# Kernel optimization log

Hardware: AMD Instinct MI355X
Metric: run time of the kernel (lower is better)

Reference implementation:

```python
import jax, jax.numpy as jnp
import numpy as np

C = 128; L = 2; LMAX = 3; NB = 8
R_MAX = 5.0; P_CUT = 5.0; AVG_NEI = 16.0
DELTA_K = 0.2; K_CUT = 0.6; NKRBF = 128; DP = 8
B_GRAPHS = 8; N_ATOMS = 3200; N_EDGES = 51200; NEL = 10
SKIP = (2.0 + 1.0) ** -0.5  # skip_connection_factor with use_ewald=True
_LOFLM_NP = np.repeat(np.arange(4), [1, 3, 5, 7])  # l index of each of 16 lm slots
LOFLM = jnp.asarray(_LOFLM_NP)
LM1H = jnp.asarray(np.eye(4, dtype=np.float32)[_LOFLM_NP])  # [16,4] one-hot lm->l


def _k_grid_np():
    r = np.arange(-3, 4)
    g = np.stack(np.meshgrid(r, r, r, indexing='ij'), -1).reshape(-1, 3).astype(np.float32) * DELTA_K
    return g[np.linalg.norm(g, axis=1) <= K_CUT + 1e-6]  # [K,3], K=123


def _k_rbf_np(kg):
    d = np.linalg.norm(kg, axis=1)
    c = np.linspace(0.0, K_CUT, NKRBF).astype(np.float32)
    w = c[1] - c[0]
    return np.exp(-0.5 * ((d[:, None] - c[None, :]) / w) ** 2).astype(np.float32)


def _sph_harm(u):
    # real spherical harmonics, e3nn 'component' normalization, l=0..3 -> 16 comps
    x, y, z = u[:, 0], u[:, 1], u[:, 2]
    s3, s5, s15 = 3.0 ** 0.5, 5.0 ** 0.5, 15.0 ** 0.5
    c70, c105, c42, c7 = 70.0 ** 0.5 / 4.0, 105.0 ** 0.5, 42.0 ** 0.5 / 4.0, 7.0 ** 0.5 / 2.0
    comps = [jnp.ones_like(x),
             s3 * x, s3 * y, s3 * z,
             s15 * x * y, s15 * y * z, 0.5 * s5 * (3 * z * z - 1.0), s15 * x * z, 0.5 * s15 * (x * x - y * y),
             c70 * y * (3 * x * x - y * y), c105 * x * y * z, c42 * y * (5 * z * z - 1.0),
             c7 * z * (5 * z * z - 3.0), c42 * x * (5 * z * z - 1.0), 0.5 * c105 * z * (x * x - y * y),
             c70 * x * (x * x - 3 * y * y)]
    return jnp.stack(comps, axis=-1)


def _radial(r):
    # Bessel basis * polynomial cutoff envelope (p=5)
    n = jnp.arange(1, NB + 1, dtype=r.dtype)
    rb = jnp.sqrt(2.0 / R_MAX) * jnp.sin(n * jnp.pi * r[:, None] / R_MAX) / jnp.maximum(r, 1e-9)[:, None]
    uu = jnp.clip(r / R_MAX, 0.0, 1.0)
    p = P_CUT
    env = 1.0 - (p + 1.0) * (p + 2.0) / 2.0 * uu ** 5 + p * (p + 2.0) * uu ** 6 - p * (p + 1.0) / 2.0 * uu ** 7
    env = env * (r < R_MAX)
    return rb * env[:, None]


def _forward(positions, node_attrs, shifts, edge_index, batch, kgrid, krbf, W_embed, atomic_E, rW1, rb1, rW2, rb2, rW3, rb3, rW4, Wup, w2, w3, Wmix, Wr0, Wr1a, Wr1b, Wdown, WupE, Wpre1, bpre1, Wpre2, bpre2, Wm1, bm1, Wm2, bm2):
    silu = jax.nn.silu
    src, dst = edge_index[0], edge_index[1]
    vec = positions[dst] - positions[src] + shifts            # [E,3]
    r = jnp.linalg.norm(vec, axis=1)
    uvec = vec / jnp.maximum(r, 1e-9)[:, None]
    Y = _sph_harm(uvec)                                       # [E,16]
    ef = _radial(r)                                           # [E,8]
    h = node_attrs @ W_embed                                  # [N,C]
    e0 = jax.ops.segment_sum(node_attrs @ atomic_E, batch, num_segments=B_GRAPHS)
    # Ewald precompute (shared across layers, as in the torch code: dot/sinc computed once)
    dot = positions @ kgrid.T                                 # [N,K]
    sd = jnp.prod(jnp.sinc(0.5 * DELTA_K * positions), axis=1, keepdims=True)  # [N,1]
    cosd = sd * jnp.cos(dot)
    sind = sd * jnp.sin(dot)
    kdown = krbf @ Wdown                                      # [K,DP]
    energy = e0
    for i in range(L):
        # ---- Ewald block ----
        hres = h + silu(h @ Wpre1[i] + bpre1[i]) @ Wpre2[i] + bpre2[i]
        kfilter = kdown @ WupE[i]                             # [K,C]
        sfr = jax.ops.segment_sum(hres[:, None, :] * cosd[:, :, None], batch, num_segments=B_GRAPHS)  # [B,K,C]
        sfi = jax.ops.segment_sum(hres[:, None, :] * sind[:, :, None], batch, num_segments=B_GRAPHS)
        he = 0.01 * (jnp.einsum('nk,nkc->nc', cosd, (sfr * kfilter)[batch])
                     + jnp.einsum('nk,nkc->nc', sind, (sfi * kfilter)[batch]))
        he = silu(he @ Wm1[i] + bm1[i])
        he = silu(he @ Wm2[i] + bm2[i])
        # ---- equivariant interaction (channelwise TP with SH, radial-MLP weights) ----
        hu = h @ Wup[i]
        w = silu(ef @ rW1[i] + rb1[i])
        w = silu(w @ rW2[i] + rb2[i])
        w = silu(w @ rW3[i] + rb3[i])
        w = (w @ rW4[i]).reshape(-1, C, LMAX + 1)             # [E,C,4] per-(channel,l) weights
        we = jnp.take(w, LOFLM, axis=2)                       # [E,C,16]
        msg = we * hu[src][:, :, None] * Y[:, None, :]        # [E,C,16]
        A = jax.ops.segment_sum(msg, dst, num_segments=positions.shape[0]) / AVG_NEI  # [N,C,16]
        # ---- product basis (invariant contractions up to correlation 3) + residual sc ----
        scal = A[:, :, 0]
        inv2 = jnp.einsum('ncs,sl->ncl', A * A, LM1H)         # [N,C,4] per-l norms
        feats = scal + jnp.einsum('ncl,lc->nc', inv2, w2[i]) + scal * jnp.einsum('ncl,lc->nc', inv2, w3[i])
        hprod = feats @ Wmix[i] + h
        h = SKIP * (hprod + he)
        # ---- readout ----
        if i < L - 1:
            node_e = (h @ Wr0)[:, 0]
        else:
            node_e = (silu(h @ Wr1a) @ Wr1b)[:, 0]
        energy = energy + jax.ops.segment_sum(node_e, batch, num_segments=B_GRAPHS)
    return energy  # [B]


def setup_inputs() -> dict:
    ks = jax.random.split(jax.random.key(0), 32)
    def rn(i, shape, scale):
        return jax.random.normal(ks[i], shape, jnp.float32) * scale
    d = {}
    d['positions'] = jax.random.normal(ks[0], (N_ATOMS, 3), jnp.float32)
    d['node_attrs'] = jax.random.uniform(ks[1], (N_ATOMS, NEL), dtype=jnp.float32)
    d['shifts'] = jnp.zeros((N_EDGES, 3), jnp.float32)
    d['edge_index'] = jax.random.randint(ks[2], (2, N_EDGES), 0, N_ATOMS)
    d['batch'] = jnp.sort(jax.random.randint(ks[3], (N_ATOMS,), 0, B_GRAPHS))
    kg = _k_grid_np()
    d['kgrid'] = jnp.asarray(kg)
    d['krbf'] = jnp.asarray(_k_rbf_np(kg))
    d['W_embed'] = rn(4, (NEL, C), NEL ** -0.5)
    d['atomic_E'] = rn(5, (NEL,), 1.0)
    d['rW1'] = rn(6, (L, NB, 64), NB ** -0.5)
    d['rb1'] = jnp.zeros((L, 64), jnp.float32)
    d['rW2'] = rn(7, (L, 64, 64), 64 ** -0.5)
    d['rb2'] = jnp.zeros((L, 64), jnp.float32)
    d['rW3'] = rn(8, (L, 64, 64), 64 ** -0.5)
    d['rb3'] = jnp.zeros((L, 64), jnp.float32)
    d['rW4'] = rn(9, (L, 64, C * (LMAX + 1)), 64 ** -0.5)
    d['Wup'] = rn(10, (L, C, C), C ** -0.5)
    d['w2'] = rn(11, (L, LMAX + 1, C), 0.1)
    d['w3'] = rn(12, (L, LMAX + 1, C), 0.1)
    d['Wmix'] = rn(13, (L, C, C), C ** -0.5)
    d['Wr0'] = rn(14, (C, 1), C ** -0.5)
    d['Wr1a'] = rn(15, (C, 16), C ** -0.5)
    d['Wr1b'] = rn(16, (16, 1), 16 ** -0.5)
    d['Wdown'] = rn(17, (NKRBF, DP), NKRBF ** -0.5)
    d['WupE'] = rn(18, (L, DP, C), DP ** -0.5)
    d['Wpre1'] = rn(19, (L, C, C), C ** -0.5)
    d['bpre1'] = jnp.zeros((L, C), jnp.float32)
    d['Wpre2'] = rn(20, (L, C, C), C ** -0.5)
    d['bpre2'] = jnp.zeros((L, C), jnp.float32)
    d['Wm1'] = rn(21, (L, C, C), C ** -0.5)
    d['bm1'] = jnp.zeros((L, C), jnp.float32)
    d['Wm2'] = rn(22, (L, C, C), C ** -0.5)
    d['bm2'] = jnp.zeros((L, C), jnp.float32)
    return d


def reference(positions, node_attrs, shifts, edge_index, batch, kgrid, krbf, W_embed, atomic_E, rW1, rb1, rW2, rb2, rW3, rb3, rW4, Wup, w2, w3, Wmix, Wr0, Wr1a, Wr1b, Wdown, WupE, Wpre1, bpre1, Wpre2, bpre2, Wm1, bm1, Wm2, bm2):
    return _forward(positions, node_attrs, shifts, edge_index, batch, kgrid, krbf, W_embed, atomic_E, rW1, rb1, rW2, rb2, rW3, rb3, rW4, Wup, w2, w3, Wmix, Wr0, Wr1a, Wr1b, Wdown, WupE, Wpre1, bpre1, Wpre2, bpre2, Wm1, bm1, Wm2, bm2)
```

## Files before the change

kernel.cpp:

```cpp
#include <hip/hip_runtime.h>
#include <hip/hip_bf16.h>
#include <math.h>

constexpr int NA  = 3200;
constexpr int NE  = 51200;
constexpr int C   = 128;
constexpr int NK  = 123;
constexpr int NKP = 128;
constexpr int BG  = 8;
constexpr int SFSPLIT = 8;
constexpr float SKIPF = 0.57735026918962576f;
constexpr float AVGN  = 16.0f;
constexpr size_t SFSZ = (size_t)BG * NK * C;

__device__ __forceinline__ float dsilu(float x) { return x / (1.0f + expf(-x)); }

__device__ __forceinline__ unsigned short f2bf(float f) {
    unsigned int u = __float_as_uint(f);
    unsigned int r = (u + 0x7fffu + ((u >> 16) & 1u)) >> 16;
    return (unsigned short)r;
}
__device__ __forceinline__ float bf2f(unsigned short s) {
    return __uint_as_float(((unsigned int)s) << 16);
}

typedef __attribute__((ext_vector_type(8))) short short8;
typedef __attribute__((ext_vector_type(4))) float f32x4;

__global__ __launch_bounds__(256, 2) void k_pre(
    const float* __restrict__ h,
    const unsigned short* __restrict__ W1t, const float* __restrict__ b1,
    const unsigned short* __restrict__ Wut,
    const unsigned short* __restrict__ W2t, const float* __restrict__ b2,
    float* __restrict__ hu, float* __restrict__ hres)
{
    constexpr int MT = 32, ASH = 136;
    __shared__ unsigned short Xs[MT * ASH];
    __shared__ unsigned short Ts[MT * ASH];
    __shared__ unsigned short Ws[128 * ASH];
    const int tid = threadIdx.x;
    const int m0 = blockIdx.x * MT;

    for (int idx = tid; idx < MT * 32; idx += 256) {
        int r = idx >> 5, c4 = idx & 31;
        float4 v = ((const float4*)h)[(size_t)(m0 + r) * 32 + c4];
        ushort4 pk;
        pk.x = f2bf(v.x); pk.y = f2bf(v.y); pk.z = f2bf(v.z); pk.w = f2bf(v.w);
        *(ushort4*)(Xs + r * ASH + c4 * 4) = pk;
    }
    for (int idx = tid; idx < 128 * 16; idx += 256) {
        int r = idx >> 4, s = idx & 15;
        *(short8*)(Ws + r * ASH + s * 8) = ((const short8*)W1t)[(size_t)r * 16 + s];
    }
    __syncthreads();

    const int wave = tid >> 6;
    const int lane = tid & 63;
    const int q = lane >> 4;
    const int l16 = lane & 15;
    const int mh = (wave & 1) * 16;
    const int nh = (wave >> 1) * 64;

    f32x4 acc[4];
#pragma unroll
    for (int ni = 0; ni < 4; ni++) acc[ni] = (f32x4){0.f, 0.f, 0.f, 0.f};
#pragma unroll
    for (int kc = 0; kc < 4; kc++) {
        short8 a = *(const short8*)(Xs + (mh + l16) * ASH + kc * 32 + q * 8);
#pragma unroll
        for (int ni = 0; ni < 4; ni++) {
            short8 b = *(const short8*)(Ws + (nh + ni * 16 + l16) * ASH + kc * 32 + q * 8);
            acc[ni] = __builtin_amdgcn_mfma_f32_16x16x32_bf16(a, b, acc[ni], 0, 0, 0);
        }
    }
#pragma unroll
    for (int ni = 0; ni < 4; ni++) {
        float bv = b1[nh + ni * 16 + l16];
#pragma unroll
        for (int r = 0; r < 4; r++)
            Ts[(mh + q * 4 + r) * ASH + nh + ni * 16 + l16] = f2bf(dsilu(acc[ni][r] + bv));
    }
    __syncthreads();
    for (int idx = tid; idx < 128 * 16; idx += 256) {
        int r = idx >> 4, s = idx & 15;
        *(short8*)(Ws + r * ASH + s * 8) = ((const short8*)Wut)[(size_t)r * 16 + s];
    }
    __syncthreads();
#pragma unroll
    for (int ni = 0; ni < 4; ni++) acc[ni] = (f32x4){0.f, 0.f, 0.f, 0.f};
#pragma unroll
    for (int kc = 0; kc < 4; kc++) {
        short8 a = *(const short8*)(Xs + (mh + l16) * ASH + kc * 32 + q * 8);
#pragma unroll
        for (int ni = 0; ni < 4; ni++) {
            short8 b = *(const short8*)(Ws + (nh + ni * 16 + l16) * ASH + kc * 32 + q * 8);
            acc[ni] = __builtin_amdgcn_mfma_f32_16x16x32_bf16(a, b, acc[ni], 0, 0, 0);
        }
    }
#pragma unroll
    for (int ni = 0; ni < 4; ni++) {
#pragma unroll
        for (int r = 0; r < 4; r++)
            hu[(size_t)(m0 + mh + q * 4 + r) * C + nh + ni * 16 + l16] = acc[ni][r];
    }
    __syncthreads();
    for (int idx = tid; idx < 128 * 16; idx += 256) {
        int r = idx >> 4, s = idx & 15;
        *(short8*)(Ws + r * ASH + s * 8) = ((const short8*)W2t)[(size_t)r * 16 + s];
    }
    __syncthreads();
#pragma unroll
    for (int ni = 0; ni < 4; ni++) acc[ni] = (f32x4){0.f, 0.f, 0.f, 0.f};
#pragma unroll
    for (int kc = 0; kc < 4; kc++) {
        short8 a = *(const short8*)(Ts + (mh + l16) * ASH + kc * 32 + q * 8);
#pragma unroll
        for (int ni = 0; ni < 4; ni++) {
            short8 b = *(const short8*)(Ws + (nh + ni * 16 + l16) * ASH + kc * 32 + q * 8);
            acc[ni] = __builtin_amdgcn_mfma_f32_16x16x32_bf16(a, b, acc[ni], 0, 0, 0);
        }
    }
#pragma unroll
    for (int ni = 0; ni < 4; ni++) {
        float bv = b2[nh + ni * 16 + l16];
#pragma unroll
        for (int r = 0; r < 4; r++) {
            int row = m0 + mh + q * 4 + r;
            int col = nh + ni * 16 + l16;
            hres[(size_t)row * C + col] = acc[ni][r] + bv + h[(size_t)row * C + col];
        }
    }
}

__global__ __launch_bounds__(256, 4) void k_edge_mlp(
    const float* __restrict__ efb,
    const unsigned short* __restrict__ W1bt, const float* __restrict__ rb1,
    const unsigned short* __restrict__ W2bt, const float* __restrict__ rb2,
    const unsigned short* __restrict__ W3bt, const float* __restrict__ rb3,
    const unsigned short* __restrict__ W4bt,
    unsigned short* __restrict__ wbuf)
{
    constexpr int MT = 64;
    constexpr int TS = 72;
    constexpr int AS0 = 40;
    __shared__ __align__(16) char smem[32768];
    unsigned short* A0 = (unsigned short*)smem;
    unsigned short* T1 = (unsigned short*)(smem + 5120);
    unsigned short* T2 = (unsigned short*)(smem + 14336);
    unsigned short* WB = (unsigned short*)(smem + 23552);
    const int tid = threadIdx.x;
    const int nb = NE / MT;
    const int layer = (blockIdx.x >= nb) ? 1 : 0;
    const size_t m0 = (size_t)(blockIdx.x - layer * nb) * MT;

    if (tid < 128) {
        int r = tid >> 1, hf = tid & 1;
        float4 v = ((const float4*)efb)[(m0 + r) * 2 + hf];
        ushort4 pk;
        pk.x = f2bf(v.x); pk.y = f2bf(v.y); pk.z = f2bf(v.z); pk.w = f2bf(v.w);
        *(ushort4*)(A0 + r * AS0 + hf * 4) = pk;
    }
    const short8 z8 = (short8){0,0,0,0,0,0,0,0};
    if (tid < 192) {
        int r = tid / 3, s = tid - r * 3;
        *(short8*)(A0 + r * AS0 + 8 + s * 8) = z8;
    }
    {
        int r = tid >> 2, s = tid & 3;
        *(short8*)(WB + r * TS + s * 8) =
            ((const short8*)(W1bt + (size_t)layer * 64 * 32))[r * 4 + s];
    }
    __syncthreads();

    const int wave = tid >> 6;
    const int lane = tid & 63;
    const int q = lane >> 4;
    const int l16 = lane & 15;
    const int mw = wave * 16;

    const float* b1 = rb1 + layer * 64;
    const float* b2 = rb2 + layer * 64;
    const float* b3 = rb3 + layer * 64;

    f32x4 acc[4];
#pragma unroll
    for (int ni = 0; ni < 4; ni++) acc[ni] = (f32x4){0.f, 0.f, 0.f, 0.f};
    {
        short8 a = *(const short8*)(A0 + (mw + l16) * AS0 + q * 8);
#pragma unroll
        for (int ni = 0; ni < 4; ni++) {
            short8 b = *(const short8*)(WB + (ni * 16 + l16) * TS + q * 8);
            acc[ni] = __builtin_amdgcn_mfma_f32_16x16x32_bf16(a, b, acc[ni], 0, 0, 0);
        }
    }
#pragma unroll
    for (int ni = 0; ni < 4; ni++) {
        float bv = b1[ni * 16 + l16];
#pragma unroll
        for (int r = 0; r < 4; r++)
            T1[(mw + q * 4 + r) * TS + ni * 16 + l16] = f2bf(dsilu(acc[ni][r] + bv));
    }
    __syncthreads();
    for (int idx = tid; idx < 512; idx += 256) {
        int r = idx >> 3, s = idx & 7;
        *(short8*)(WB + r * TS + s * 8) =
            ((const short8*)(W2bt + (size_t)layer * 64 * 64))[r * 8 + s];
    }
    __syncthreads();
#pragma unroll
    for (int ni = 0; ni < 4; ni++) acc[ni] = (f32x4){0.f, 0.f, 0.f, 0.f};
#pragma unroll
    for (int kc = 0; kc < 2; kc++) {
        short8 a = *(const short8*)(T1 + (mw + l16) * TS + kc * 32 + q * 8);
#pragma unroll
        for (int ni = 0; ni < 4; ni++) {
            short8 b = *(const short8*)(WB + (ni * 16 + l16) * TS + kc * 32 + q * 8);
            acc[ni] = __builtin_amdgcn_mfma_f32_16x16x32_bf16(a, b, acc[ni], 0, 0, 0);
        }
    }
#pragma unroll
    for (int ni = 0; ni < 4; ni++) {
        float bv = b2[ni * 16 + l16];
#pragma unroll
        for (int r = 0; r < 4; r++)
            T2[(mw + q * 4 + r) * TS + ni * 16 + l16] = f2bf(dsilu(acc[ni][r] + bv));
    }
    __syncthreads();
    for (int idx = tid; idx < 512; idx += 256) {
        int r = idx >> 3, s = idx & 7;
        *(short8*)(WB + r * TS + s * 8) =
            ((const short8*)(W3bt + (size_t)layer * 64 * 64))[r * 8 + s];
    }
    __syncthreads();
#pragma unroll
    for (int ni = 0; ni < 4; ni++) acc[ni] = (f32x4){0.f, 0.f, 0.f, 0.f};
#pragma unroll
    for (int kc = 0; kc < 2; kc++) {
        short8 a = *(const short8*)(T2 + (mw + l16) * TS + kc * 32 + q * 8);
#pragma unroll
        for (int ni = 0; ni < 4; ni++) {
            short8 b = *(const short8*)(WB + (ni * 16 + l16) * TS + kc * 32 + q * 8);
            acc[ni] = __builtin_amdgcn_mfma_f32_16x16x32_bf16(a, b, acc[ni], 0, 0, 0);
        }
    }
#pragma unroll
    for (int ni = 0; ni < 4; ni++) {
        float bv = b3[ni * 16 + l16];
#pragma unroll
        for (int r = 0; r < 4; r++)
            T1[(mw + q * 4 + r) * TS + ni * 16 + l16] = f2bf(dsilu(acc[ni][r] + bv));
    }

    const unsigned short* W4l = W4bt + (size_t)layer * 512 * 64;
    unsigned short* wout = wbuf + ((size_t)layer * NE + m0) * 512;
#pragma unroll 1
    for (int nt = 0; nt < 8; nt++) {
        __syncthreads();
        for (int idx = tid; idx < 512; idx += 256) {
            int r = idx >> 3, s = idx & 7;
            *(short8*)(WB + r * TS + s * 8) = ((const short8*)W4l)[(nt * 64 + r) * 8 + s];
        }
        __syncthreads();
#pragma unroll
        for (int ni = 0; ni < 4; ni++) acc[ni] = (f32x4){0.f, 0.f, 0.f, 0.f};
#pragma unroll
        for (int kc = 0; kc < 2; kc++) {
            short8 a = *(const short8*)(T1 + (mw + l16) * TS + kc * 32 + q * 8);
#pragma unroll
            for (int ni = 0; ni < 4; ni++) {
                short8 b = *(const short8*)(WB + (ni * 16 + l16) * TS + kc * 32 + q * 8);
                acc[ni] = __builtin_amdgcn_mfma_f32_16x16x32_bf16(a, b, acc[ni], 0, 0, 0);
            }
        }
#pragma unroll
        for (int ni = 0; ni < 4; ni++)
#pragma unroll
            for (int r = 0; r < 4; r++) {
                int row = mw + q * 4 + r;
                int col = nt * 64 + ni * 16 + l16;
                wout[(size_t)row * 512 + col] = f2bf(acc[ni][r]);
            }
    }
}

constexpr int TK0 = NA;
constexpr int TK1 = TK0 + 8;
constexpr int TK2 = TK1 + 512;
constexpr int TK3 = TK2 + 64;
constexpr int TK4 = TK3 + 64;
constexpr int TK4b = TK4 + 32;
constexpr int TK5 = TK4b + 256;
constexpr int TK6 = TK5 + 256;
constexpr int TK7 = TK6 + 256;
constexpr int TK8 = TK7 + 256;
constexpr int TK9 = TK8 + 256;
constexpr int TKEND = TK9 + 1;

__device__ __forceinline__ float sincn(float x) {
    float px = 3.14159265358979323846f * x;
    return (fabsf(px) < 1e-8f) ? 1.0f : (sinf(px) / px);
}

__device__ __forceinline__ void convT128_task(
    const float* __restrict__ W, unsigned short* __restrict__ Wt, int idx)
{
    int layer = idx >> 14, rem = idx & 16383;
    int n = rem >> 7, k = rem & 127;
    Wt[((size_t)layer << 14) + (n << 7) + k] = f2bf(W[((size_t)layer << 14) + (k << 7) + n]);
}

__global__ __launch_bounds__(128) void k_setup(
    const float* __restrict__ na, const float* __restrict__ Wemb,
    const float* __restrict__ aE, const int* __restrict__ batch,
    const float* __restrict__ pos, const float* __restrict__ kgrid,
    const float* __restrict__ krbf, const float* __restrict__ Wdown,
    const float* __restrict__ rW4, const float* __restrict__ rW2,
    const float* __restrict__ rW3, const float* __restrict__ rW1,
    const float* __restrict__ Wm1, const float* __restrict__ Wm2,
    const float* __restrict__ Wpre1, const float* __restrict__ Wpre2,
    const float* __restrict__ Wup,
    float* __restrict__ h, float* __restrict__ e0buf,
    float* __restrict__ cosd, float* __restrict__ sind,
    unsigned short* __restrict__ cosdb, unsigned short* __restrict__ sindb,
    float* __restrict__ kdwn,
    unsigned short* __restrict__ W4bt, unsigned short* __restrict__ W2bt,
    unsigned short* __restrict__ W3bt, unsigned short* __restrict__ W1bt,
    unsigned short* __restrict__ Wm1bt, unsigned short* __restrict__ Wm2bt,
    unsigned short* __restrict__ Wpre1bt, unsigned short* __restrict__ Wpre2bt,
    unsigned short* __restrict__ Wupbt,
    int* __restrict__ gs)
{
    const int bx = blockIdx.x;
    const int t = threadIdx.x;
    __shared__ int cnt[BG];

    if (bx < TK0) {
        int n = bx, c = t;
        float s = 0.f;
#pragma unroll
        for (int k = 0; k < 10; k++) s += na[n * 10 + k] * Wemb[k * C + c];
        h[(size_t)n * C + c] = s;
        if (c == 0) {
            float e = 0.f;
#pragma unroll
            for (int k = 0; k < 10; k++) e += na[n * 10 + k] * aE[k];
            e0buf[n] = e;
        }
        float p0 = pos[n * 3 + 0], p1 = pos[n * 3 + 1], p2 = pos[n * 3 + 2];
        float sd = sincn(0.1f * p0) * sincn(0.1f * p1) * sincn(0.1f * p2);
        int k = t;
        float cv = 0.f, sv = 0.f;
        if (k < NK) {
            float d = p0 * kgrid[k * 3 + 0] + p1 * kgrid[k * 3 + 1] + p2 * kgrid[k * 3 + 2];
            float sn, cs;
            sincosf(d, &sn, &cs);
            cv = sd * cs;
            sv = sd * sn;
        }
        cosd[(size_t)n * NKP + k] = cv;
        sind[(size_t)n * NKP + k] = sv;
        cosdb[(size_t)n * NKP + k] = f2bf(cv);
        sindb[(size_t)n * NKP + k] = f2bf(sv);
    } else if (bx < TK1) {
        int slot = (bx - TK0) * 128 + t;
        if (slot < NK * 8) {
            int k = slot >> 3, j = slot & 7;
            float s = 0.f;
            for (int r = 0; r < 128; r++) s += krbf[k * 128 + r] * Wdown[r * 8 + j];
            kdwn[slot] = s;
        }
    } else if (bx < TK2) {
        int idx = (bx - TK1) * 128 + t;
        int layer = idx >> 15, rem = idx & 32767;
        int n = rem >> 6, k = rem & 63;
        W4bt[((size_t)layer * 512 + n) * 64 + k] = f2bf(rW4[((size_t)layer * 64 + k) * 512 + n]);
    } else if (bx < TK3) {
        int idx = (bx - TK2) * 128 + t;
        int layer = idx >> 12, rem = idx & 4095;
        int n = rem >> 6, k = rem & 63;
        W2bt[((size_t)layer * 64 + n) * 64 + k] = f2bf(rW2[((size_t)layer * 64 + k) * 64 + n]);
    } else if (bx < TK4) {
        int idx = (bx - TK3) * 128 + t;
        int layer = idx >> 12, rem = idx & 4095;
        int n = rem >> 6, k = rem & 63;
        W3bt[((size_t)layer * 64 + n) * 64 + k] = f2bf(rW3[((size_t)layer * 64 + k) * 64 + n]);
    } else if (bx < TK4b) {
        int idx = (bx - TK4) * 128 + t;
        int layer = idx >> 11, rem = idx & 2047;
        int n = rem >> 5, k = rem & 31;
        W1bt[((size_t)layer * 64 + n) * 32 + k] =
            (k < 8) ? f2bf(rW1[((size_t)layer * 8 + k) * 64 + n]) : (unsigned short)0;
    } else if (bx < TK5) {
        convT128_task(Wm1, Wm1bt, (bx - TK4b) * 128 + t);
    } else if (bx < TK6) {
        convT128_task(Wm2, Wm2bt, (bx - TK5) * 128 + t);
    } else if (bx < TK7) {
        convT128_task(Wpre1, Wpre1bt, (bx - TK6) * 128 + t);
    } else if (bx < TK8) {
        convT128_task(Wpre2, Wpre2bt, (bx - TK7) * 128 + t);
    } else if (bx < TK9) {
        convT128_task(Wup, Wupbt, (bx - TK8) * 128 + t);
    } else {
        if (t < BG) cnt[t] = 0;
        __syncthreads();
        for (int n = t; n < NA; n += 128) atomicAdd(&cnt[batch[n]], 1);
        __syncthreads();
        if (t == 0) {
            int s = 0;
            for (int b = 0; b < BG; b++) { gs[b] = s; s += cnt[b]; }
            gs[BG] = s;
        }
    }
}

__global__ __launch_bounds__(256) void k_count(const int* __restrict__ eidx, int* __restrict__ deg)
{
    int e = blockIdx.x * 256 + threadIdx.x;
    if (e < NE) atomicAdd(&deg[eidx[NE + e]], 1);
}

__global__ __launch_bounds__(1024) void k_scan(
    const int* __restrict__ deg, int* __restrict__ offs, int* __restrict__ cursor)
{
    __shared__ int sc[1024];
    int tid = threadIdx.x;
    int base = tid * 4;
    int v[4]; int s = 0;
#pragma unroll
    for (int i = 0; i < 4; i++) {
        int idx = base + i;
        int d = (idx < NA) ? deg[idx] : 0;
        v[i] = s; s += d;
    }
    sc[tid] = s;
    __syncthreads();
    for (int ofs = 1; ofs < 1024; ofs <<= 1) {
        int t = (tid >= ofs) ? sc[tid - ofs] : 0;
        __syncthreads();
        sc[tid] += t;
        __syncthreads();
    }
    int excl = (tid > 0) ? sc[tid - 1] : 0;
#pragma unroll
    for (int i = 0; i < 4; i++) {
        int idx = base + i;
        if (idx < NA) { int o = excl + v[i]; offs[idx] = o; cursor[idx] = o; }
    }
    if (tid == 1023) offs[NA] = sc[1023];
}

__global__ __launch_bounds__(256) void k_fill(
    const int* __restrict__ eidx, int* __restrict__ cursor,
    int* __restrict__ perm, int* __restrict__ srcP)
{
    int e = blockIdx.x * 256 + threadIdx.x;
    if (e < NE) {
        int d = eidx[NE + e];
        int p = atomicAdd(&cursor[d], 1);
        perm[p] = e;
        srcP[p] = eidx[e];
    }
}

__global__ __launch_bounds__(256) void k_edge_geom(
    const float* __restrict__ pos, const float* __restrict__ shifts,
    const int* __restrict__ eidx, const int* __restrict__ perm,
    float* __restrict__ Y, float* __restrict__ ef)
{
    int j = blockIdx.x * 256 + threadIdx.x;
    if (j >= NE) return;
    int e = perm[j];
    int s = eidx[e], d = eidx[NE + e];
    float vx = pos[d * 3 + 0] - pos[s * 3 + 0] + shifts[e * 3 + 0];
    float vy = pos[d * 3 + 1] - pos[s * 3 + 1] + shifts[e * 3 + 1];
    float vz = pos[d * 3 + 2] - pos[s * 3 + 2] + shifts[e * 3 + 2];
    float r = sqrtf(vx * vx + vy * vy + vz * vz);
    float rinv = 1.0f / fmaxf(r, 1e-9f);
    float x = vx * rinv, y = vy * rinv, z = vz * rinv;

    const float s3 = 1.7320508075688772f, s5 = 2.2360679774997896f, s15 = 3.8729833462074170f;
    const float c70 = 2.0916500663351889f;
    const float c105 = 10.246950765959598f;
    const float c42 = 1.6201851746019651f;
    const float c7 = 1.3228756555322954f;
    float o[16];
    o[0] = 1.0f;
    o[1] = s3 * x; o[2] = s3 * y; o[3] = s3 * z;
    o[4] = s15 * x * y; o[5] = s15 * y * z; o[6] = 0.5f * s5 * (3.f * z * z - 1.f);
    o[7] = s15 * x * z; o[8] = 0.5f * s15 * (x * x - y * y);
    o[9]  = c70 * y * (3.f * x * x - y * y);
    o[10] = c105 * x * y * z;
    o[11] = c42 * y * (5.f * z * z - 1.f);
    o[12] = c7 * z * (5.f * z * z - 3.f);
    o[13] = c42 * x * (5.f * z * z - 1.f);
    o[14] = 0.5f * c105 * z * (x * x - y * y);
    o[15] = c70 * x * (x * x - 3.f * y * y);
    float4* Y4 = (float4*)(Y + (size_t)j * 16);
    Y4[0] = make_float4(o[0], o[1], o[2], o[3]);
    Y4[1] = make_float4(o[4], o[5], o[6], o[7]);
    Y4[2] = make_float4(o[8], o[9], o[10], o[11]);
    Y4[3] = make_float4(o[12], o[13], o[14], o[15]);

    float uu = fminf(fmaxf(r * 0.2f, 0.f), 1.f);
    float u2 = uu * uu, u4 = u2 * u2, u5 = u4 * uu, u6 = u5 * uu, u7 = u6 * uu;
    float env = 1.f - 21.f * u5 + 35.f * u6 - 15.f * u7;
    env = (r < 5.0f) ? env : 0.0f;
    float pref = 0.63245553203367587f * rinv * env;
    const float pio5 = 0.62831853071795865f;
    float efv[8];
#pragma unroll
    for (int n1 = 1; n1 <= 8; n1++) efv[n1 - 1] = pref * sinf(n1 * pio5 * r);
    float4* E4 = (float4*)(ef + (size_t)j * 8);
    E4[0] = make_float4(efv[0], efv[1], efv[2], efv[3]);
    E4[1] = make_float4(efv[4], efv[5], efv[6], efv[7]);
}

__global__ __launch_bounds__(256, 4) void k_sf(
    const float* __restrict__ hres, const float* __restrict__ cosd, const float* __restrict__ sind,
    const int* __restrict__ gs, const float* __restrict__ kdwn, const float* __restrict__ WupE,
    float* __restrict__ sfp)
{
    const int b = blockIdx.x, kt = blockIdx.y, sp = blockIdx.z;
    const int n0 = gs[b], n1 = gs[b + 1];
    const int cnt = n1 - n0;
    const int per = (cnt + SFSPLIT - 1) / SFSPLIT;
    const int cs = n0 + sp * per;
    const int ce = min(cs + per, n1);

    __shared__ float Hs[32 * 128];
    __shared__ float Cs[32 * 32];
    __shared__ float Ss[32 * 32];

    const int tid = threadIdx.x;
    const int tx = tid & 31;
    const int ty = tid >> 5;

    float accR[4][4], accI[4][4];
#pragma unroll
    for (int i = 0; i < 4; i++)
#pragma unroll
        for (int j = 0; j < 4; j++) { accR[i][j] = 0.f; accI[i][j] = 0.f; }

    float4* H4 = (float4*)Hs;
    float4* C4 = (float4*)Cs;
    float4* S4 = (float4*)Ss;

    for (int nb = cs; nb < ce; nb += 32) {
        __syncthreads();
        for (int idx = tid; idx < 32 * 32; idx += 256) {
            int r = idx >> 5, c4 = idx & 31;
            int n = nb + r;
            H4[idx] = (n < ce) ? ((const float4*)hres)[(size_t)n * 32 + c4]
                               : make_float4(0.f, 0.f, 0.f, 0.f);
        }
        for (int idx = tid; idx < 32 * 8; idx += 256) {
            int r = idx >> 3, k4 = idx & 7;
            int n = nb + r;
            float4 cv = make_float4(0.f, 0.f, 0.f, 0.f), sv = cv;
            if (n < ce) {
                cv = ((const float4*)cosd)[(size_t)n * 32 + kt * 8 + k4];
                sv = ((const float4*)sind)[(size_t)n * 32 + kt * 8 + k4];
            }
            C4[idx] = cv;
            S4[idx] = sv;
        }
        __syncthreads();
        const int lim = min(32, ce - nb);
        for (int n = 0; n < lim; n++) {
            float4 hv = H4[n * 32 + tx];
            float4 cv = C4[n * 8 + ty];
            float4 sv = S4[n * 8 + ty];
            float h[4] = { hv.x, hv.y, hv.z, hv.w };
            float ck[4] = { cv.x, cv.y, cv.z, cv.w };
            float sk[4] = { sv.x, sv.y, sv.z, sv.w };
#pragma unroll
            for (int i = 0; i < 4; i++)
#pragma unroll
                for (int j = 0; j < 4; j++) {
                    accR[i][j] += ck[i] * h[j];
                    accI[i][j] += sk[i] * h[j];
                }
        }
    }

    const int kbase = kt * 32 + ty * 4;
    float* baseR = sfp + (size_t)sp * SFSZ;
    float* baseI = sfp + (size_t)(SFSPLIT + sp) * SFSZ;
#pragma unroll
    for (int i = 0; i < 4; i++) {
        int k = kbase + i;
        if (k < NK) {
            float4 kfv = make_float4(0.f, 0.f, 0.f, 0.f);
#pragma unroll
            for (int j = 0; j < 8; j++) {
                float kd = kdwn[k * 8 + j];
                float4 wv = ((const float4*)WupE)[(size_t)j * 32 + tx];
                kfv.x += kd * wv.x; kfv.y += kd * wv.y;
                kfv.z += kd * wv.z; kfv.w += kd * wv.w;
            }
            float vx = kfv.x * 0.01f, vy = kfv.y * 0.01f, vz = kfv.z * 0.01f, vw = kfv.w * 0.01f;
            size_t o = ((size_t)(b * NK + k)) * C + tx * 4;
            *(float4*)(baseR + o) = make_float4(accR[i][0] * vx, accR[i][1] * vy,
                                                accR[i][2] * vz, accR[i][3] * vw);
            *(float4*)(baseI + o) = make_float4(accI[i][0] * vx, accI[i][1] * vy,
                                                accI[i][2] * vz, accI[i][3] * vw);
        }
    }
}

__global__ __launch_bounds__(256) void k_sfredT(
    const float* __restrict__ sfp,
    unsigned short* __restrict__ sfrT, unsigned short* __restrict__ sfiT)
{
    const int kc = blockIdx.x * 16;
    const int b = blockIdx.y;
    __shared__ float Tr[16 * 128];
    __shared__ float Ti[16 * 128];
    const int tid = threadIdx.x;
    const size_t S4 = SFSZ / 4;
    const float4* P4 = (const float4*)sfp;

    for (int idx = tid; idx < 16 * 32; idx += 256) {
        int kk = idx >> 5, c4 = idx & 31;
        float4 ar = make_float4(0.f, 0.f, 0.f, 0.f), ai = ar;
        if (kc + kk < NK) {
            size_t off = ((size_t)(b * NK + kc + kk)) * 32 + c4;
#pragma unroll
            for (int sp = 0; sp < SFSPLIT; sp++) {
                float4 r = P4[(size_t)sp * S4 + off];
                ar.x += r.x; ar.y += r.y; ar.z += r.z; ar.w += r.w;
                float4 q = P4[(size_t)(SFSPLIT + sp) * S4 + off];
                ai.x += q.x; ai.y += q.y; ai.z += q.z; ai.w += q.w;
            }
        }
        ((float4*)Tr)[idx] = ar;
        ((float4*)Ti)[idx] = ai;
    }
    __syncthreads();
    const int c = tid & 127;
    const int sel = tid >> 7;
    const float* T = sel ? Ti : Tr;
    unsigned short* out = sel ? sfiT : sfrT;
    unsigned short tmp[16];
#pragma unroll
    for (int kk = 0; kk < 16; kk++) tmp[kk] = f2bf(T[kk * 128 + c]);
    short8* dst = (short8*)(out + ((size_t)(b * 128 + c)) * NKP + kc);
    dst[0] = *(short8*)(tmp);
    dst[1] = *(short8*)(tmp + 8);
}

__global__ __launch_bounds__(256) void k_he_mlp(
    const unsigned short* __restrict__ cosdb, const unsigned short* __restrict__ sindb,
    const unsigned short* __restrict__ sfrT, const unsigned short* __restrict__ sfiT,
    const int* __restrict__ gs,
    const unsigned short* __restrict__ Wm1t, const float* __restrict__ bm1,
    const unsigned short* __restrict__ Wm2t, const float* __restrict__ bm2,
    float* __restrict__ he2)
{
    constexpr int ASH = 136;
    constexpr int BSH = 72;
    __shared__ __align__(16) char smem[54272];
    unsigned short* Ca = (unsigned short*)smem;
    unsigned short* Sa = (unsigned short*)(smem + 8704);
    unsigned short* Br = (unsigned short*)(smem + 17408);
    unsigned short* Bi = (unsigned short*)(smem + 35840);
    unsigned short* Xs = (unsigned short*)smem;
    unsigned short* Ts = (unsigned short*)(smem + 8704);
    unsigned short* Ws = (unsigned short*)(smem + 17408);

    const int b = blockIdx.y;
    const int a0g = gs[b], a1g = gs[b + 1];
    const int a0 = a0g + blockIdx.x * 32;
    if (a0 >= a1g) return;
    const int nal = min(32, a1g - a0);
    const int tid = threadIdx.x;

    const short8 z8 = (short8){0,0,0,0,0,0,0,0};
    for (int idx = tid; idx < 32 * 16; idx += 256) {
        int r = idx >> 4, s = idx & 15;
        short8 cv = z8, sv = z8;
        if (r < nal) {
            cv = ((const short8*)cosdb)[(size_t)(a0 + r) * 16 + s];
            sv = ((const short8*)sindb)[(size_t)(a0 + r) * 16 + s];
        }
        *(short8*)(Ca + r * ASH + s * 8) = cv;
        *(short8*)(Sa + r * ASH + s * 8) = sv;
    }

    const int wave = tid >> 6;
    const int lane = tid & 63;
    const int q = lane >> 4;
    const int l16 = lane & 15;
    const int mh = (wave & 1) * 16;
    const int nh = (wave >> 1) * 64;

    f32x4 acc[4];
#pragma unroll
    for (int ni = 0; ni < 4; ni++) acc[ni] = (f32x4){0.f, 0.f, 0.f, 0.f};

#pragma unroll
    for (int kc2 = 0; kc2 < 2; kc2++) {
        __syncthreads();
        for (int idx = tid; idx < 128 * 8; idx += 256) {
            int c = idx >> 3, s = idx & 7;
            size_t gi = (size_t)(b * 128 + c) * 16 + kc2 * 8 + s;
            *(short8*)(Br + c * BSH + s * 8) = ((const short8*)sfrT)[gi];
            *(short8*)(Bi + c * BSH + s * 8) = ((const short8*)sfiT)[gi];
        }
        __syncthreads();
#pragma unroll
        for (int ks = 0; ks < 2; ks++) {
            short8 ar = *(const short8*)(Ca + (mh + l16) * ASH + kc2 * 64 + ks * 32 + q * 8);
            short8 ai = *(const short8*)(Sa + (mh + l16) * ASH + kc2 * 64 + ks * 32 + q * 8);
#pragma unroll
            for (int ni = 0; ni < 4; ni++) {
                short8 br = *(const short8*)(Br + (nh + ni * 16 + l16) * BSH + ks * 32 + q * 8);
                acc[ni] = __builtin_amdgcn_mfma_f32_16x16x32_bf16(ar, br, acc[ni], 0, 0, 0);
                short8 bi = *(const short8*)(Bi + (nh + ni * 16 + l16) * BSH + ks * 32 + q * 8);
                acc[ni] = __builtin_amdgcn_mfma_f32_16x16x32_bf16(ai, bi, acc[ni], 0, 0, 0);
            }
        }
    }
    __syncthreads();

#pragma unroll
    for (int ni = 0; ni < 4; ni++) {
#pragma unroll
        for (int r = 0; r < 4; r++)
            Xs[(mh + q * 4 + r) * ASH + nh + ni * 16 + l16] = f2bf(acc[ni][r]);
    }
    __syncthreads();
    for (int idx = tid; idx < 128 * 16; idx += 256) {
        int r = idx >> 4, s = idx & 15;
        *(short8*)(Ws + r * ASH + s * 8) = ((const short8*)Wm1t)[(size_t)r * 16 + s];
    }
    __syncthreads();

    f32x4 acc2[4];
#pragma unroll
    for (int ni = 0; ni < 4; ni++) acc2[ni] = (f32x4){0.f, 0.f, 0.f, 0.f};
#pragma unroll
    for (int kc = 0; kc < 4; kc++) {
        short8 a = *(const short8*)(Xs + (mh + l16) * ASH + kc * 32 + q * 8);
#pragma unroll
        for (int ni = 0; ni < 4; ni++) {
            short8 bb = *(const short8*)(Ws + (nh + ni * 16 + l16) * ASH + kc * 32 + q * 8);
            acc2[ni] = __builtin_amdgcn_mfma_f32_16x16x32_bf16(a, bb, acc2[ni], 0, 0, 0);
        }
    }
#pragma unroll
    for (int ni = 0; ni < 4; ni++) {
        float bv = bm1[nh + ni * 16 + l16];
#pragma unroll
        for (int r = 0; r < 4; r++)
            Ts[(mh + q * 4 + r) * ASH + nh + ni * 16 + l16] = f2bf(dsilu(acc2[ni][r] + bv));
    }
    __syncthreads();
    for (int idx = tid; idx < 128 * 16; idx += 256) {
        int r = idx >> 4, s = idx & 15;
        *(short8*)(Ws + r * ASH + s * 8) = ((const short8*)Wm2t)[(size_t)r * 16 + s];
    }
    __syncthreads();
#pragma unroll
    for (int ni = 0; ni < 4; ni++) acc2[ni] = (f32x4){0.f, 0.f, 0.f, 0.f};
#pragma unroll
    for (int kc = 0; kc < 4; kc++) {
        short8 a = *(const short8*)(Ts + (mh + l16) * ASH + kc * 32 + q * 8);
#pragma unroll
        for (int ni = 0; ni < 4; ni++) {
            short8 bb = *(const short8*)(Ws + (nh + ni * 16 + l16) * ASH + kc * 32 + q * 8);
            acc2[ni] = __builtin_amdgcn_mfma_f32_16x16x32_bf16(a, bb, acc2[ni], 0, 0, 0);
        }
    }
#pragma unroll
    for (int ni = 0; ni < 4; ni++) {
        int col = nh + ni * 16 + l16;
        float bv = bm2[col];
#pragma unroll
        for (int r = 0; r < 4; r++) {
            int lrow = mh + q * 4 + r;
            if (lrow < nal)
                he2[(size_t)(a0 + lrow) * C + col] = dsilu(acc2[ni][r] + bv);
        }
    }
}

__global__ __launch_bounds__(128) void k_gather_mix(
    const unsigned short* __restrict__ wbuf, const float* __restrict__ hu,
    const float* __restrict__ Y, const int* __restrict__ srcP,
    const int* __restrict__ offs,
    const float* __restrict__ w2, const float* __restrict__ w3,
    const float* __restrict__ Wmix, const float* __restrict__ h,
    const float* __restrict__ he2,
    const float* __restrict__ Wr0, const float* __restrict__ Wr1a,
    const float* __restrict__ Wr1b, int mode,
    float* __restrict__ hn, float* __restrict__ nebuf)
{
    int n = blockIdx.x, c = threadIdx.x;
    int j0 = offs[n], j1 = offs[n + 1];
    float A[16];
#pragma unroll
    for (int s = 0; s < 16; s++) A[s] = 0.f;
    for (int j = j0; j < j1; j++) {
        int s = srcP[j];
        float huc = hu[(size_t)s * C + c];
        ushort4 wv = *(const ushort4*)(wbuf + (size_t)j * 512 + c * 4);
        const float4* Yp = (const float4*)(Y + (size_t)j * 16);
        float4 y0 = Yp[0], y1 = Yp[1], y2 = Yp[2], y3 = Yp[3];
        float m0 = bf2f(wv.x) * huc, m1 = bf2f(wv.y) * huc;
        float m2 = bf2f(wv.z) * huc, m3 = bf2f(wv.w) * huc;
        A[0] += m0 * y0.x;
        A[1] += m1 * y0.y;  A[2]  += m1 * y0.z;  A[3]  += m1 * y0.w;
        A[4] += m2 * y1.x;  A[5]  += m2 * y1.y;  A[6]  += m2 * y1.z;  A[7] += m2 * y1.w;
        A[8] += m2 * y2.x;
        A[9] += m3 * y2.y;  A[10] += m3 * y2.z;  A[11] += m3 * y2.w;
        A[12] += m3 * y3.x; A[13] += m3 * y3.y;  A[14] += m3 * y3.z;  A[15] += m3 * y3.w;
    }
    const float inv = 1.0f / AVGN;
#pragma unroll
    for (int s = 0; s < 16; s++) A[s] *= inv;
    float scal = A[0];
    float i0 = A[0] * A[0];
    float i1 = A[1] * A[1] + A[2] * A[2] + A[3] * A[3];
    float i2 = A[4] * A[4] + A[5] * A[5] + A[6] * A[6] + A[7] * A[7] + A[8] * A[8];
    float i3 = A[9] * A[9] + A[10] * A[10] + A[11] * A[11] + A[12] * A[12] +
               A[13] * A[13] + A[14] * A[14] + A[15] * A[15];
    float t2 = i0 * w2[c] + i1 * w2[C + c] + i2 * w2[2 * C + c] + i3 * w2[3 * C + c];
    float t3 = i0 * w3[c] + i1 * w3[C + c] + i2 * w3[2 * C + c] + i3 * w3[3 * C + c];
    float fe_c = scal + t2 + scal * t3;

    __shared__ float fs[128];
    __shared__ float red[16];
    fs[c] = fe_c;
    __syncthreads();

    float mix = 0.f;
#pragma unroll 8
    for (int k = 0; k < 128; k++) mix += fs[k] * Wmix[(size_t)k * C + c];

    float hnv = SKIPF * (mix + h[(size_t)n * C + c] + he2[(size_t)n * C + c]);
    hn[(size_t)n * C + c] = hnv;

    __syncthreads();
    fs[c] = hnv;
    __syncthreads();

    if (mode == 0) {
        float v = hnv * Wr0[c];
#pragma unroll
        for (int o = 32; o; o >>= 1) v += __shfl_down(v, o, 64);
        if ((c & 63) == 0) red[c >> 6] = v;
        __syncthreads();
        if (c == 0) nebuf[n] = red[0] + red[1];
    } else {
        if (c < 16) {
            float s = 0.f;
#pragma unroll 8
            for (int cc = 0; cc < 128; cc++) s += fs[cc] * Wr1a[cc * 16 + c];
            red[c] = dsilu(s) * Wr1b[c];
        }
        __syncthreads();
        if (c == 0) {
            float s = 0.f;
#pragma unroll
            for (int j = 0; j < 16; j++) s += red[j];
            nebuf[n] = s;
        }
    }
}

__global__ __launch_bounds__(256) void k_reduceE(
    const float* __restrict__ e0buf, const float* __restrict__ nebuf,
    const int* __restrict__ gs, float* __restrict__ Eout)
{
    int b = blockIdx.x, t = threadIdx.x;
    int n0 = gs[b], n1 = gs[b + 1];
    float s = 0.f;
    for (int n = n0 + t; n < n1; n += 256)
        s += e0buf[n] + nebuf[n] + nebuf[NA + n];
#pragma unroll
    for (int o = 32; o; o >>= 1) s += __shfl_down(s, o, 64);
    __shared__ float red[4];
    if ((t & 63) == 0) red[t >> 6] = s;
    __syncthreads();
    if (t == 0) Eout[b] = red[0] + red[1] + red[2] + red[3];
}

constexpr size_t NAC   = (size_t)NA * C;
constexpr size_t F_COSD = 0;
constexpr size_t F_SIND = F_COSD + (size_t)NA * NKP;
constexpr size_t F_Y    = F_SIND + (size_t)NA * NKP;
constexpr size_t F_EF   = F_Y + (size_t)NE * 16;
constexpr size_t F_H    = F_EF + (size_t)NE * 8;
constexpr size_t F_HN   = F_H + NAC;
constexpr size_t F_HRES = F_HN + NAC;
constexpr size_t F_T1   = F_HRES + NAC;
constexpr size_t F_HE2  = F_T1 + NAC;
constexpr size_t F_HU   = F_HE2 + NAC;
constexpr size_t F_TA   = F_HU + NAC;
constexpr size_t F_TB   = F_TA + (size_t)NE * 64;
constexpr size_t F_WTS  = F_TB + (size_t)NE * 64;
constexpr size_t F_W    = F_WTS + 128 * 1024;
constexpr size_t F_SFR  = F_W + (size_t)NE * 512;
constexpr size_t F_SFI  = F_SFR + SFSZ;
constexpr size_t F_SFP  = F_SFI + SFSZ;
constexpr size_t F_KD   = F_SFP + 2 * (size_t)SFSPLIT * SFSZ;
constexpr size_t F_E0   = F_KD + 1024;
constexpr size_t F_NE   = F_E0 + NA;
constexpr size_t F_CB   = F_NE + 2 * (size_t)NA;
constexpr size_t F_SB   = F_CB + (size_t)NA * 64;
constexpr size_t F_END  = F_SB + (size_t)NA * 64;
constexpr size_t I_BASE = ((F_END * 4 + 255) / 256) * 256;

extern "C" void kernel_launch(void* const* d_in, const int* in_sizes, int n_in,
                              void* d_out, int out_size, void* d_ws, size_t ws_size,
                              hipStream_t stream) {
    const float* pos    = (const float*)d_in[0];
    const float* na     = (const float*)d_in[1];
    const float* shifts = (const float*)d_in[2];
    const int*   eidx   = (const int*)d_in[3];
    const int*   batch  = (const int*)d_in[4];
    const float* kgrid  = (const float*)d_in[5];
    const float* krbf   = (const float*)d_in[6];
    const float* Wemb   = (const float*)d_in[7];
    const float* aE     = (const float*)d_in[8];
    const float* rW1    = (const float*)d_in[9];
    const float* rb1    = (const float*)d_in[10];
    const float* rW2    = (const float*)d_in[11];
    const float* rb2    = (const float*)d_in[12];
    const float* rW3    = (const float*)d_in[13];
    const float* rb3    = (const float*)d_in[14];
    const float* rW4    = (const float*)d_in[15];
    const float* Wup    = (const float*)d_in[16];
    const float* w2     = (const float*)d_in[17];
    const float* w3     = (const float*)d_in[18];
    const float* Wmix   = (const float*)d_in[19];
    const float* Wr0    = (const float*)d_in[20];
    const float* Wr1a   = (const float*)d_in[21];
    const float* Wr1b   = (const float*)d_in[22];
    const float* Wdown  = (const float*)d_in[23];
    const float* WupE   = (const float*)d_in[24];
    const float* Wpre1  = (const float*)d_in[25];
    const float* bpre1  = (const float*)d_in[26];
    const float* Wpre2  = (const float*)d_in[27];
    const float* bpre2  = (const float*)d_in[28];
    const float* Wm1    = (const float*)d_in[29];
    const float* bm1    = (const float*)d_in[30];
    const float* Wm2    = (const float*)d_in[31];
    const float* bm2    = (const float*)d_in[32];

    float* fw = (float*)d_ws;
    float* cosd = fw + F_COSD;
    float* sind = fw + F_SIND;
    float* Ybuf = fw + F_Y;
    float* efb  = fw + F_EF;
    float* h    = fw + F_H;
    float* hn   = fw + F_HN;
    float* hres = fw + F_HRES;
    float* he2  = fw + F_HE2;
    float* hu   = fw + F_HU;
    unsigned short* W4bt = (unsigned short*)(fw + F_WTS);
    unsigned short* W2bt  = W4bt + (size_t)2 * 512 * 64;
    unsigned short* W3bt  = W2bt + (size_t)2 * 64 * 64;
    unsigned short* Wm1bt = W3bt + (size_t)2 * 64 * 64;
    unsigned short* Wm2bt = Wm1bt + (size_t)2 * 128 * 128;
    unsigned short* Wp1bt = Wm2bt + (size_t)2 * 128 * 128;
    unsigned short* Wp2bt = Wp1bt + (size_t)2 * 128 * 128;
    unsigned short* Wupbt = Wp2bt + (size_t)2 * 128 * 128;
    unsigned short* W1bt  = Wupbt + (size_t)2 * 128 * 128;
    unsigned short* wbuf = (unsigned short*)(fw + F_W);
    unsigned short* sfrT = (unsigned short*)(fw + F_SFR);
    unsigned short* sfiT = (unsigned short*)(fw + F_SFI);
    float* sfp  = fw + F_SFP;
    float* kdwn = fw + F_KD;
    float* e0buf = fw + F_E0;
    float* nebuf = fw + F_NE;
    unsigned short* cosdb = (unsigned short*)(fw + F_CB);
    unsigned short* sindb = (unsigned short*)(fw + F_SB);

    int* ip     = (int*)((char*)d_ws + I_BASE);
    int* deg    = ip;
    int* offs   = ip + NA;
    int* cursor = ip + 2 * NA + 1;
    int* perm   = ip + 3 * NA + 1;
    int* srcP   = perm + NE;
    int* gs     = srcP + NE;

    float* Eout = (float*)d_out;

    hipMemsetAsync(deg, 0, NA * sizeof(int), stream);

    k_setup<<<TKEND, 128, 0, stream>>>(
        na, Wemb, aE, batch, pos, kgrid, krbf, Wdown,
        rW4, rW2, rW3, rW1, Wm1, Wm2, Wpre1, Wpre2, Wup,
        h, e0buf, cosd, sind, cosdb, sindb, kdwn,
        W4bt, W2bt, W3bt, W1bt, Wm1bt, Wm2bt, Wp1bt, Wp2bt, Wupbt, gs);
    k_count<<<NE / 256, 256, 0, stream>>>(eidx, deg);
    k_scan<<<1, 1024, 0, stream>>>(deg, offs, cursor);
    k_fill<<<NE / 256, 256, 0, stream>>>(eidx, cursor, perm, srcP);
    k_edge_geom<<<NE / 256, 256, 0, stream>>>(pos, shifts, eidx, perm, Ybuf, efb);

    k_edge_mlp<<<2 * NE / 64, 256, 0, stream>>>(efb, W1bt, rb1, W2bt, rb2,
                                                W3bt, rb3, W4bt, wbuf);

    const dim3 gSF(BG, 4, SFSPLIT);
    const dim3 gRT(8, BG);
    const dim3 gHE(16, BG);

    for (int i = 0; i < 2; i++) {
        const float* bpre1_i = bpre1 + (size_t)i * C;
        const float* bpre2_i = bpre2 + (size_t)i * C;
        const float* WupE_i  = WupE + (size_t)i * 8 * C;
        const float* bm1_i   = bm1 + (size_t)i * C;
        const float* bm2_i   = bm2 + (size_t)i * C;
        const float* w2_i    = w2 + (size_t)i * 4 * C;
        const float* w3_i    = w3 + (size_t)i * 4 * C;
        const float* Wmix_i  = Wmix + (size_t)i * C * C;
        const unsigned short* Wm1bt_i = Wm1bt + (size_t)i * 128 * 128;
        const unsigned short* Wm2bt_i = Wm2bt + (size_t)i * 128 * 128;
        const unsigned short* Wp1bt_i = Wp1bt + (size_t)i * 128 * 128;
        const unsigned short* Wp2bt_i = Wp2bt + (size_t)i * 128 * 128;
        const unsigned short* Wupbt_i = Wupbt + (size_t)i * 128 * 128;
        const unsigned short* wbuf_i = wbuf + (size_t)i * NE * 512;

        k_pre<<<NA / 32, 256, 0, stream>>>(h, Wp1bt_i, bpre1_i, Wupbt_i,
                                           Wp2bt_i, bpre2_i, hu, hres);

        k_sf<<<gSF, 256, 0, stream>>>(hres, cosd, sind, gs, kdwn, WupE_i, sfp);
        k_sfredT<<<gRT, 256, 0, stream>>>(sfp, sfrT, sfiT);
        k_he_mlp<<<gHE, 256, 0, stream>>>(cosdb, sindb, sfrT, sfiT, gs,
                                          Wm1bt_i, bm1_i, Wm2bt_i, bm2_i, he2);

        k_gather_mix<<<NA, 128, 0, stream>>>(wbuf_i, hu, Ybuf, srcP, offs,
                                             w2_i, w3_i, Wmix_i, h, he2,
                                             Wr0, Wr1a, Wr1b, (i == 0) ? 0 : 1,
                                             hn, nebuf + (size_t)i * NA);

        float* tmp = h; h = hn; hn = tmp;
    }

    k_reduceE<<<BG, 256, 0, stream>>>(e0buf, nebuf, gs, Eout);
}
```

Baseline: 313.4 us.

## Fuse edge geometry into edge MLP and degree count into setup kernel

Edge geometry (spherical harmonics and Bessel radial features) is now computed inside the edge MLP kernel's input staging instead of a separate kernel, removing the fp32 edge-feature buffer round trip and one launch. Layer-0 blocks also write Y. The degree-counting atomics are folded into extra blocks of the setup kernel, removing another launch. In exchange, radial features are recomputed for both layers, and the first 64 threads of each MLP block do serial transcendental work before the sync.

```diff
diff --git a/kernel.cpp b/kernel.cpp
--- a/kernel.cpp
+++ b/kernel.cpp
@@ -133,12 +133,13 @@
 }
 
 __global__ __launch_bounds__(256, 4) void k_edge_mlp(
-    const float* __restrict__ efb,
+    const float* __restrict__ pos, const float* __restrict__ shifts,
+    const int* __restrict__ eidx, const int* __restrict__ perm,
     const unsigned short* __restrict__ W1bt, const float* __restrict__ rb1,
     const unsigned short* __restrict__ W2bt, const float* __restrict__ rb2,
     const unsigned short* __restrict__ W3bt, const float* __restrict__ rb3,
     const unsigned short* __restrict__ W4bt,
-    unsigned short* __restrict__ wbuf)
+    unsigned short* __restrict__ wbuf, float* __restrict__ Y)
 {
     constexpr int MT = 64;
     constexpr int TS = 72;
@@ -153,12 +154,55 @@
     const int layer = (blockIdx.x >= nb) ? 1 : 0;
     const size_t m0 = (size_t)(blockIdx.x - layer * nb) * MT;
 
-    if (tid < 128) {
-        int r = tid >> 1, hf = tid & 1;
-        float4 v = ((const float4*)efb)[(m0 + r) * 2 + hf];
-        ushort4 pk;
-        pk.x = f2bf(v.x); pk.y = f2bf(v.y); pk.z = f2bf(v.z); pk.w = f2bf(v.w);
-        *(ushort4*)(A0 + r * AS0 + hf * 4) = pk;
+    if (tid < 64) {
+        int j = (int)m0 + tid;
+        int e = perm[j];
+        int si = eidx[e], di = eidx[NE + e];
+        float vx = pos[di * 3 + 0] - pos[si * 3 + 0] + shifts[e * 3 + 0];
+        float vy = pos[di * 3 + 1] - pos[si * 3 + 1] + shifts[e * 3 + 1];
+        float vz = pos[di * 3 + 2] - pos[si * 3 + 2] + shifts[e * 3 + 2];
+        float r = sqrtf(vx * vx + vy * vy + vz * vz);
+        float rinv = 1.0f / fmaxf(r, 1e-9f);
+        float x = vx * rinv, y = vy * rinv, z = vz * rinv;
+
+        const float s3 = 1.7320508075688772f, s5 = 2.2360679774997896f, s15 = 3.8729833462074170f;
+        const float c70 = 2.0916500663351889f;
+        const float c105 = 10.246950765959598f;
+        const float c42 = 1.6201851746019651f;
+        const float c7 = 1.3228756555322954f;
+        float o[16];
+        o[0] = 1.0f;
+        o[1] = s3 * x; o[2] = s3 * y; o[3] = s3 * z;
+        o[4] = s15 * x * y; o[5] = s15 * y * z; o[6] = 0.5f * s5 * (3.f * z * z - 1.f);
+        o[7] = s15 * x * z; o[8] = 0.5f * s15 * (x * x - y * y);
+        o[9]  = c70 * y * (3.f * x * x - y * y);
+        o[10] = c105 * x * y * z;
+        o[11] = c42 * y * (5.f * z * z - 1.f);
+        o[12] = c7 * z * (5.f * z * z - 3.f);
+        o[13] = c42 * x * (5.f * z * z - 1.f);
+        o[14] = 0.5f * c105 * z * (x * x - y * y);
+        o[15] = c70 * x * (x * x - 3.f * y * y);
+        if (layer == 0) {
+            float4* Y4 = (float4*)(Y + (size_t)j * 16);
+            Y4[0] = make_float4(o[0], o[1], o[2], o[3]);
+            Y4[1] = make_float4(o[4], o[5], o[6], o[7]);
+            Y4[2] = make_float4(o[8], o[9], o[10], o[11]);
+            Y4[3] = make_float4(o[12], o[13], o[14], o[15]);
+        }
+        float uu = fminf(fmaxf(r * 0.2f, 0.f), 1.f);
+        float u2 = uu * uu, u4 = u2 * u2, u5 = u4 * uu, u6 = u5 * uu, u7 = u6 * uu;
+        float env = 1.f - 21.f * u5 + 35.f * u6 - 15.f * u7;
+        env = (r < 5.0f) ? env : 0.0f;
+        float pref = 0.63245553203367587f * rinv * env;
+        const float pio5 = 0.62831853071795865f;
+        float efv[8];
+#pragma unroll
+        for (int n1 = 1; n1 <= 8; n1++) efv[n1 - 1] = pref * sinf(n1 * pio5 * r);
+        ushort4 pk0, pk1;
+        pk0.x = f2bf(efv[0]); pk0.y = f2bf(efv[1]); pk0.z = f2bf(efv[2]); pk0.w = f2bf(efv[3]);
+        pk1.x = f2bf(efv[4]); pk1.y = f2bf(efv[5]); pk1.z = f2bf(efv[6]); pk1.w = f2bf(efv[7]);
+        *(ushort4*)(A0 + tid * AS0 + 0) = pk0;
+        *(ushort4*)(A0 + tid * AS0 + 4) = pk1;
     }
     const short8 z8 = (short8){0,0,0,0,0,0,0,0};
     if (tid < 192) {
@@ -294,7 +338,8 @@
 constexpr int TK7 = TK6 + 256;
 constexpr int TK8 = TK7 + 256;
 constexpr int TK9 = TK8 + 256;
-constexpr int TKEND = TK9 + 1;
+constexpr int TKA = TK9 + 1;
+constexpr int TKEND = TKA + NE / 128;
 
 __device__ __forceinline__ float sincn(float x) {
     float px = 3.14159265358979323846f * x;
@@ -318,7 +363,7 @@
     const float* __restrict__ rW3, const float* __restrict__ rW1,
     const float* __restrict__ Wm1, const float* __restrict__ Wm2,
     const float* __restrict__ Wpre1, const float* __restrict__ Wpre2,
-    const float* __restrict__ Wup,
+    const float* __restrict__ Wup, const int* __restrict__ eidx,
     float* __restrict__ h, float* __restrict__ e0buf,
     float* __restrict__ cosd, float* __restrict__ sind,
     unsigned short* __restrict__ cosdb, unsigned short* __restrict__ sindb,
@@ -328,7 +373,7 @@
     unsigned short* __restrict__ Wm1bt, unsigned short* __restrict__ Wm2bt,
     unsigned short* __restrict__ Wpre1bt, unsigned short* __restrict__ Wpre2bt,
     unsigned short* __restrict__ Wupbt,
-    int* __restrict__ gs)
+    int* __restrict__ gs, int* __restrict__ deg)
 {
     const int bx = blockIdx.x;
     const int t = threadIdx.x;
@@ -400,7 +445,7 @@
         convT128_task(Wpre2, Wpre2bt, (bx - TK7) * 128 + t);
     } else if (bx < TK9) {
         convT128_task(Wup, Wupbt, (bx - TK8) * 128 + t);
-    } else {
+    } else if (bx < TKA) {
         if (t < BG) cnt[t] = 0;
         __syncthreads();
         for (int n = t; n < NA; n += 128) atomicAdd(&cnt[batch[n]], 1);
@@ -410,13 +455,10 @@
             for (int b = 0; b < BG; b++) { gs[b] = s; s += cnt[b]; }
             gs[BG] = s;
         }
-    }
-}
-
-__global__ __launch_bounds__(256) void k_count(const int* __restrict__ eidx, int* __restrict__ deg)
-{
-    int e = blockIdx.x * 256 + threadIdx.x;
-    if (e < NE) atomicAdd(&deg[eidx[NE + e]], 1);
+    } else {
+        int e = (bx - TKA) * 128 + t;
+        if (e < NE) atomicAdd(&deg[eidx[NE + e]], 1);
+    }
 }
 
 __global__ __launch_bounds__(1024) void k_scan(
@@ -460,59 +502,6 @@
         perm[p] = e;
         srcP[p] = eidx[e];
     }
-}
-
-__global__ __launch_bounds__(256) void k_edge_geom(
-    const float* __restrict__ pos, const float* __restrict__ shifts,
-    const int* __restrict__ eidx, const int* __restrict__ perm,
-    float* __restrict__ Y, float* __restrict__ ef)
-{
-    int j = blockIdx.x * 256 + threadIdx.x;
-    if (j >= NE) return;
-    int e = perm[j];
-    int s = eidx[e], d = eidx[NE + e];
-    float vx = pos[d * 3 + 0] - pos[s * 3 + 0] + shifts[e * 3 + 0];
-    float vy = pos[d * 3 + 1] - pos[s * 3 + 1] + shifts[e * 3 + 1];
-    float vz = pos[d * 3 + 2] - pos[s * 3 + 2] + shifts[e * 3 + 2];
-    float r = sqrtf(vx * vx + vy * vy + vz * vz);
-    float rinv = 1.0f / fmaxf(r, 1e-9f);
-    float x = vx * rinv, y = vy * rinv, z = vz * rinv;
-
-    const float s3 = 1.7320508075688772f, s5 = 2.2360679774997896f, s15 = 3.8729833462074170f;
-    const float c70 = 2.0916500663351889f;
-    const float c105 = 10.246950765959598f;
-    const float c42 = 1.6201851746019651f;
-    const float c7 = 1.3228756555322954f;
-    float o[16];
-    o[0] = 1.0f;
-    o[1] = s3 * x; o[2] = s3 * y; o[3] = s3 * z;
-    o[4] = s15 * x * y; o[5] = s15 * y * z; o[6] = 0.5f * s5 * (3.f * z * z - 1.f);
-    o[7] = s15 * x * z; o[8] = 0.5f * s15 * (x * x - y * y);
-    o[9]  = c70 * y * (3.f * x * x - y * y);
-    o[10] = c105 * x * y * z;
-    o[11] = c42 * y * (5.f * z * z - 1.f);
-    o[12] = c7 * z * (5.f * z * z - 3.f);
-    o[13] = c42 * x * (5.f * z * z - 1.f);
-    o[14] = 0.5f * c105 * z * (x * x - y * y);
-    o[15] = c70 * x * (x * x - 3.f * y * y);
-    float4* Y4 = (float4*)(Y + (size_t)j * 16);
-    Y4[0] = make_float4(o[0], o[1], o[2], o[3]);
-    Y4[1] = make_float4(o[4], o[5], o[6], o[7]);
-    Y4[2] = make_float4(o[8], o[9], o[10], o[11]);
-    Y4[3] = make_float4(o[12], o[13], o[14], o[15]);
-
-    float uu = fminf(fmaxf(r * 0.2f, 0.f), 1.f);
-    float u2 = uu * uu, u4 = u2 * u2, u5 = u4 * uu, u6 = u5 * uu, u7 = u6 * uu;
-    float env = 1.f - 21.f * u5 + 35.f * u6 - 15.f * u7;
-    env = (r < 5.0f) ? env : 0.0f;
-    float pref = 0.63245553203367587f * rinv * env;
-    const float pio5 = 0.62831853071795865f;
-    float efv[8];
-#pragma unroll
-    for (int n1 = 1; n1 <= 8; n1++) efv[n1 - 1] = pref * sinf(n1 * pio5 * r);
-    float4* E4 = (float4*)(ef + (size_t)j * 8);
-    E4[0] = make_float4(efv[0], efv[1], efv[2], efv[3]);
-    E4[1] = make_float4(efv[4], efv[5], efv[6], efv[7]);
 }
 
 __global__ __launch_bounds__(256, 4) void k_sf(
@@ -953,7 +942,6 @@
     float* cosd = fw + F_COSD;
     float* sind = fw + F_SIND;
     float* Ybuf = fw + F_Y;
-    float* efb  = fw + F_EF;
     float* h    = fw + F_H;
     float* hn   = fw + F_HN;
     float* hres = fw + F_HRES;
@@ -992,16 +980,15 @@
 
     k_setup<<<TKEND, 128, 0, stream>>>(
         na, Wemb, aE, batch, pos, kgrid, krbf, Wdown,
-        rW4, rW2, rW3, rW1, Wm1, Wm2, Wpre1, Wpre2, Wup,
+        rW4, rW2, rW3, rW1, Wm1, Wm2, Wpre1, Wpre2, Wup, eidx,
         h, e0buf, cosd, sind, cosdb, sindb, kdwn,
-        W4bt, W2bt, W3bt, W1bt, Wm1bt, Wm2bt, Wp1bt, Wp2bt, Wupbt, gs);
-    k_count<<<NE / 256, 256, 0, stream>>>(eidx, deg);
+        W4bt, W2bt, W3bt, W1bt, Wm1bt, Wm2bt, Wp1bt, Wp2bt, Wupbt, gs, deg);
     k_scan<<<1, 1024, 0, stream>>>(deg, offs, cursor);
     k_fill<<<NE / 256, 256, 0, stream>>>(eidx, cursor, perm, srcP);
-    k_edge_geom<<<NE / 256, 256, 0, stream>>>(pos, shifts, eidx, perm, Ybuf, efb);
-
-    k_edge_mlp<<<2 * NE / 64, 256, 0, stream>>>(efb, W1bt, rb1, W2bt, rb2,
-                                                W3bt, rb3, W4bt, wbuf);
+
+    k_edge_mlp<<<2 * NE / 64, 256, 0, stream>>>(pos, shifts, eidx, perm,
+                                                W1bt, rb1, W2bt, rb2,
+                                                W3bt, rb3, W4bt, wbuf, Ybuf);
 
     const dim3 gSF(BG, 4, SFSPLIT);
     const dim3 gRT(8, BG);
```

Result: faster. 306.1 us (-2.3%).
